# Optimization experiments

Hardware: AMD Instinct MI355X
Metric: run time of the kernel (lower is better)

Reference implementation:

```python
import jax, jax.numpy as jnp
import numpy as np

B, T, E, H, D = 4, 1024, 1024, 16, 64


def rel_shift(x):
    # x: [B, H, T1, T2] -> Transformer-XL relative shift
    b, h, t1, t2 = x.shape
    x = jnp.pad(x, ((0, 0), (0, 0), (0, 0), (1, 0)))  # pad zeros on left of last dim
    x = x.reshape(b, h, t2 + 1, t1)[:, :, 1:]
    return x.reshape(b, h, t1, t2)


def setup_inputs() -> dict:
    key = jax.random.key(0)
    ks = jax.random.split(key, 9)
    s = 0.02
    return {
        "x": jax.random.normal(ks[0], (B, T, E), jnp.float32),
        "pos": jax.random.normal(ks[1], (1, T, E), jnp.float32),
        "Wq": jax.random.normal(ks[2], (E, H, D), jnp.float32) * s,
        "Wk": jax.random.normal(ks[3], (E, H, D), jnp.float32) * s,
        "Wv": jax.random.normal(ks[4], (E, H, D), jnp.float32) * s,
        "Wr": jax.random.normal(ks[5], (E, H, D), jnp.float32) * s,
        "r_w_bias": jax.random.normal(ks[6], (1, H, 1, D), jnp.float32) * s,
        "r_r_bias": jax.random.normal(ks[7], (1, H, 1, D), jnp.float32) * s,
        "merge_W": jax.random.normal(ks[8], (E, E), jnp.float32) * s,
        "merge_b": jnp.zeros((E,), jnp.float32),
    }


def reference(x, pos, Wq, Wk, Wv, Wr, r_w_bias, r_r_bias, merge_W, merge_b):
    d = Wq.shape[-1]
    scale = d ** -0.5
    # per-head linear projections via einsum (MultiHeadLinear)
    q = jnp.einsum('bte,ehd->bhtd', x, Wq) * scale   # [B,H,T,D]
    k = jnp.einsum('bte,ehd->bhtd', x, Wk)           # [B,H,T,D]
    v = jnp.einsum('bte,ehd->bhtd', x, Wv)           # [B,H,T,D]
    r = jnp.einsum('upe,ehd->uhpd', pos, Wr)[0]      # [H,P,D], P == T

    # content logits: (q + u) . k
    content_logits = jnp.einsum('bhtd,bhsd->bhts', q + r_w_bias, k)
    # relative logits: (q + v_bias) . rel_keys, then rel_shift
    relative_logits = jnp.einsum('bhtd,hpd->bhtp', q + r_r_bias, r)
    relative_logits = rel_shift(relative_logits)

    logits = content_logits + relative_logits        # [B,H,T,T]
    weights = jax.nn.softmax(logits, axis=-1)
    # attend and merge heads: [B,T,H,D] -> [B,T,E]
    attended = jnp.einsum('bhts,bhsd->bthd', weights, v).reshape(x.shape[0], x.shape[1], -1)
    return attended @ merge_W + merge_b
```

## Files before the change

### kernel.cpp

```cpp
#include <hip/hip_runtime.h>
#include <hip/hip_bf16.h>

#define BB 4
#define TT 1024
#define EE 1024
#define HH 16
#define DD 64

typedef unsigned short ushort_t;
typedef unsigned int uint_t;
typedef __attribute__((ext_vector_type(8))) short short8;
typedef __attribute__((ext_vector_type(4))) float f32x4;

__device__ __forceinline__ ushort_t f2bf(float f) {
  uint_t u = __float_as_uint(f);
  u += 0x7fffu + ((u >> 16) & 1u);
  return (ushort_t)(u >> 16);
}
__device__ __forceinline__ float bf2f(ushort_t s) {
  return __uint_as_float(((uint_t)s) << 16);
}

__device__ __forceinline__ void gload16(const ushort_t* src, ushort_t* dst) {
  __builtin_amdgcn_global_load_lds(
      (const __attribute__((address_space(1))) void*)src,
      (__attribute__((address_space(3))) void*)dst, 16, 0, 0);
}

__global__ void __launch_bounds__(256) conv_flat(
    const float* __restrict__ in, ushort_t* __restrict__ out, int n) {
  int i = (blockIdx.x * 256 + threadIdx.x) * 8;
  if (i >= n) return;
  float4 a = *(const float4*)(in + i);
  float4 b = *(const float4*)(in + i + 4);
  uint4 o;
  o.x = (uint_t)f2bf(a.x) | ((uint_t)f2bf(a.y) << 16);
  o.y = (uint_t)f2bf(a.z) | ((uint_t)f2bf(a.w) << 16);
  o.z = (uint_t)f2bf(b.x) | ((uint_t)f2bf(b.y) << 16);
  o.w = (uint_t)f2bf(b.z) | ((uint_t)f2bf(b.w) << 16);
  *(uint4*)(out + i) = o;
}

__global__ void __launch_bounds__(256) trans_conv4(
    const float* __restrict__ W0, const float* __restrict__ W1,
    const float* __restrict__ W2, const float* __restrict__ W3,
    ushort_t* __restrict__ O0, ushort_t* __restrict__ O1,
    ushort_t* __restrict__ O2, ushort_t* __restrict__ O3) {
  const float* W; ushort_t* Oh;
  switch (blockIdx.z) {
    case 0: W = W0; Oh = O0; break;
    case 1: W = W1; Oh = O1; break;
    case 2: W = W2; Oh = O2; break;
    default: W = W3; Oh = O3; break;
  }
  __shared__ float Ts[64][65];
  const int n0 = blockIdx.x * 64, k0 = blockIdx.y * 64;
  const int t = threadIdx.x;
  const int r = t >> 2, cs = (t & 3) * 16;
  const float* src = W + (size_t)(k0 + r) * 1024 + n0 + cs;
  #pragma unroll
  for (int e = 0; e < 16; e += 4) {
    float4 v4 = *(const float4*)(src + e);
    Ts[r][cs + e] = v4.x; Ts[r][cs + e + 1] = v4.y;
    Ts[r][cs + e + 2] = v4.z; Ts[r][cs + e + 3] = v4.w;
  }
  __syncthreads();
  ushort_t hb[16];
  #pragma unroll
  for (int e = 0; e < 16; e++) hb[e] = f2bf(Ts[cs + e][r]);
  ushort_t* dh = Oh + (size_t)(n0 + r) * 1024 + k0 + cs;
  *(uint4*)dh = *(const uint4*)hb;
  *(uint4*)(dh + 8) = *(const uint4*)(hb + 8);
}

__global__ void __launch_bounds__(256) trans_conv(
    const float* __restrict__ W, ushort_t* __restrict__ Oh,
    ushort_t* __restrict__ Ol) {
  __shared__ float Ts[64][65];
  const int n0 = blockIdx.x * 64, k0 = blockIdx.y * 64;
  const int t = threadIdx.x;
  const int r = t >> 2, cs = (t & 3) * 16;
  const float* src = W + (size_t)(k0 + r) * 1024 + n0 + cs;
  #pragma unroll
  for (int e = 0; e < 16; e += 4) {
    float4 v4 = *(const float4*)(src + e);
    Ts[r][cs + e] = v4.x; Ts[r][cs + e + 1] = v4.y;
    Ts[r][cs + e + 2] = v4.z; Ts[r][cs + e + 3] = v4.w;
  }
  __syncthreads();
  ushort_t hb[16], lb[16];
  #pragma unroll
  for (int e = 0; e < 16; e++) {
    float v = Ts[cs + e][r];
    hb[e] = f2bf(v);
    lb[e] = f2bf(v - bf2f(hb[e]));
  }
  ushort_t* dh = Oh + (size_t)(n0 + r) * 1024 + k0 + cs;
  *(uint4*)dh = *(const uint4*)hb;
  *(uint4*)(dh + 8) = *(const uint4*)(hb + 8);
  ushort_t* dl = Ol + (size_t)(n0 + r) * 1024 + k0 + cs;
  *(uint4*)dl = *(const uint4*)lb;
  *(uint4*)(dl + 8) = *(const uint4*)(lb + 8);
}

__global__ void __launch_bounds__(256) mfma_gemm_proj(
    const ushort_t* __restrict__ A,
    const ushort_t* __restrict__ B0, const ushort_t* __restrict__ B1,
    const ushort_t* __restrict__ B2,
    ushort_t* __restrict__ o_qu, ushort_t* __restrict__ o_qv,
    ushort_t* __restrict__ o_k, ushort_t* __restrict__ o_v,
    const float* __restrict__ bias_u, const float* __restrict__ bias_v,
    int mode) {
  __shared__ ushort_t sA[2][128 * 32];
  __shared__ ushort_t sB[2][128 * 32];
  const int tid = threadIdx.x;
  const int w = tid >> 6, lane = tid & 63, g = lane >> 4, cl = lane & 15;
  const int wr = w >> 1, wc = w & 1;

  int widx, n0l;
  const ushort_t* Bt;
  if (mode == 0) {
    widx = blockIdx.x >> 3;
    n0l = (blockIdx.x & 7) * 128;
    Bt = (widx == 0) ? B0 : ((widx == 1) ? B1 : B2);
  } else {
    widx = 3;
    n0l = blockIdx.x * 128;
    Bt = B0;
  }
  const int m0 = blockIdx.y * 128;

  f32x4 acc[4][4];
  #pragma unroll
  for (int fi = 0; fi < 4; fi++)
    #pragma unroll
    for (int fj = 0; fj < 4; fj++) acc[fi][fj] = (f32x4){0.f, 0.f, 0.f, 0.f};

  auto STAGE = [&](int buf, int t) {
    const int k0b = t * 64;
    #pragma unroll
    for (int i = 0; i < 2; i++) {
      int cb = w * 128 + i * 64;
      int c = cb + lane;
      const char* sa = (const char*)A + (size_t)(m0 + (c >> 2)) * 2048 + k0b + (c & 3) * 16;
      gload16((const ushort_t*)sa, &sA[buf][cb * 8]);
      const char* sb = (const char*)Bt + (size_t)(n0l + (c >> 2)) * 2048 + k0b + (c & 3) * 16;
      gload16((const ushort_t*)sb, &sB[buf][cb * 8]);
    }
  };

  STAGE(0, 0);
  __syncthreads();
  int cur = 0;
  for (int t = 0; t < 32; t++) {
    if (t + 1 < 32) STAGE(cur ^ 1, t + 1);
    short8 af[4], bfr[4];
    #pragma unroll
    for (int f = 0; f < 4; f++) {
      af[f] = *(const short8*)&sA[cur][(wr * 64 + f * 16 + cl) * 32 + g * 8];
      bfr[f] = *(const short8*)&sB[cur][(wc * 64 + f * 16 + cl) * 32 + g * 8];
    }
    #pragma unroll
    for (int fi = 0; fi < 4; fi++)
      #pragma unroll
      for (int fj = 0; fj < 4; fj++)
        acc[fi][fj] = __builtin_amdgcn_mfma_f32_16x16x32_bf16(af[fi], bfr[fj], acc[fi][fj], 0, 0, 0);
    __syncthreads();
    cur ^= 1;
  }

  #pragma unroll
  for (int fi = 0; fi < 4; fi++)
    #pragma unroll
    for (int fj = 0; fj < 4; fj++)
      #pragma unroll
      for (int reg = 0; reg < 4; reg++) {
        int m = m0 + wr * 64 + fi * 16 + 4 * g + reg;
        int n = n0l + wc * 64 + fj * 16 + cl;
        float val = acc[fi][fj][reg];
        int h = n >> 6, d = n & 63;
        if (mode == 0) {
          int b = m >> 10, tt = m & 1023;
          if (widx == 0) {
            size_t idx = (((size_t)(b * HH + h)) * TT + tt) * DD + d;
            float s = val * 0.125f;
            o_qu[idx] = f2bf(s + bias_u[n]);
            o_qv[idx] = f2bf(s + bias_v[n]);
          } else if (widx == 1) {
            size_t idx = (((size_t)(b * HH + h)) * TT + tt) * DD + d;
            o_k[idx] = f2bf(val);
          } else {
            size_t idx = (((size_t)(b * HH + h)) * DD + d) * TT + tt;
            o_v[idx] = f2bf(val);
          }
        } else {
          size_t idx = ((size_t)h * TT + m) * DD + d;
          o_qu[idx] = f2bf(val);
        }
      }
}

__global__ void __launch_bounds__(256) mfma_gemm_merge(
    const ushort_t* __restrict__ Ah, const ushort_t* __restrict__ Al,
    const ushort_t* __restrict__ Bh, const ushort_t* __restrict__ Bl,
    const float* __restrict__ bias, float* __restrict__ out) {
  __shared__ ushort_t sAh[2][128 * 32], sAl[2][128 * 32];
  __shared__ ushort_t sBh[2][128 * 32], sBl[2][128 * 32];
  const int tid = threadIdx.x;
  const int w = tid >> 6, lane = tid & 63, g = lane >> 4, cl = lane & 15;
  const int wr = w >> 1, wc = w & 1;
  const int n0l = blockIdx.x * 128;
  const int m0 = blockIdx.y * 128;

  f32x4 acc[4][4];
  #pragma unroll
  for (int fi = 0; fi < 4; fi++)
    #pragma unroll
    for (int fj = 0; fj < 4; fj++) acc[fi][fj] = (f32x4){0.f, 0.f, 0.f, 0.f};

  auto STAGE = [&](int buf, int t) {
    const int k0b = t * 64;
    #pragma unroll
    for (int i = 0; i < 2; i++) {
      int cb = w * 128 + i * 64;
      int c = cb + lane;
      size_t offA = (size_t)(m0 + (c >> 2)) * 2048 + k0b + (c & 3) * 16;
      size_t offB = (size_t)(n0l + (c >> 2)) * 2048 + k0b + (c & 3) * 16;
      gload16((const ushort_t*)((const char*)Ah + offA), &sAh[buf][cb * 8]);
      gload16((const ushort_t*)((const char*)Al + offA), &sAl[buf][cb * 8]);
      gload16((const ushort_t*)((const char*)Bh + offB), &sBh[buf][cb * 8]);
      gload16((const ushort_t*)((const char*)Bl + offB), &sBl[buf][cb * 8]);
    }
  };

  STAGE(0, 0);
  __syncthreads();
  int cur = 0;
  for (int t = 0; t < 32; t++) {
    if (t + 1 < 32) STAGE(cur ^ 1, t + 1);
    short8 ah[4], al[4], bh[4], bl[4];
    #pragma unroll
    for (int f = 0; f < 4; f++) {
      int ra = (wr * 64 + f * 16 + cl) * 32 + g * 8;
      int rb = (wc * 64 + f * 16 + cl) * 32 + g * 8;
      ah[f] = *(const short8*)&sAh[cur][ra];
      al[f] = *(const short8*)&sAl[cur][ra];
      bh[f] = *(const short8*)&sBh[cur][rb];
      bl[f] = *(const short8*)&sBl[cur][rb];
    }
    #pragma unroll
    for (int fi = 0; fi < 4; fi++)
      #pragma unroll
      for (int fj = 0; fj < 4; fj++) {
        acc[fi][fj] = __builtin_amdgcn_mfma_f32_16x16x32_bf16(ah[fi], bh[fj], acc[fi][fj], 0, 0, 0);
        acc[fi][fj] = __builtin_amdgcn_mfma_f32_16x16x32_bf16(al[fi], bh[fj], acc[fi][fj], 0, 0, 0);
        acc[fi][fj] = __builtin_amdgcn_mfma_f32_16x16x32_bf16(ah[fi], bl[fj], acc[fi][fj], 0, 0, 0);
      }
    __syncthreads();
    cur ^= 1;
  }

  #pragma unroll
  for (int fi = 0; fi < 4; fi++)
    #pragma unroll
    for (int fj = 0; fj < 4; fj++)
      #pragma unroll
      for (int reg = 0; reg < 4; reg++) {
        int m = m0 + wr * 64 + fi * 16 + 4 * g + reg;
        int n = n0l + wc * 64 + fj * 16 + cl;
        out[(size_t)m * 1024 + n] = acc[fi][fj][reg] + bias[n];
      }
}

__device__ __forceinline__ void stage8s(ushort_t* region, const ushort_t* grow0,
                                        int rstride, int r0, int lane) {
  int flat16 = r0 * 8 + lane;
  int row = flat16 >> 3;
  int ch = flat16 & 7;
  const ushort_t* src = grow0 + (size_t)row * rstride + ((((ch << 4) ^ ((row & 7) << 4))) >> 1);
  gload16(src, region + r0 * 64);
}

__device__ __forceinline__ short8 ldsw(const ushort_t* base, int row, int offB) {
  const char* p = (const char*)base + row * 128 + (offB ^ ((row & 7) << 4));
  return *(const short8*)p;
}

__global__ void __launch_bounds__(256, 3) attn_mfma_kernel(
    const ushort_t* __restrict__ qu_g, const ushort_t* __restrict__ qv_g,
    const ushort_t* __restrict__ k_g, const ushort_t* __restrict__ vt_g,
    const ushort_t* __restrict__ r_g,
    ushort_t* __restrict__ att_h, ushort_t* __restrict__ att_l)
{
    __shared__ ushort_t sK[2][64 * 64];
    __shared__ ushort_t sVt[2][64 * 64];
    __shared__ ushort_t sG[4][2304];

    const int tid = threadIdx.x;
    const int w = tid >> 6;
    const int lane = tid & 63;
    const int g = lane >> 4;
    const int cl = lane & 15;

    const int lid = blockIdx.x + 16 * blockIdx.y + 256 * blockIdx.z;
    const int xcd = lid & 7, seq = lid >> 3;
    const int bhg = xcd * 8 + (seq >> 4);
    const int i0 = (seq & 15) * 64;
    const int h = bhg & 15;
    const int b = bhg >> 4;
    const size_t base_bh = ((size_t)(b * HH + h)) * TT * DD;
    const ushort_t* rh = r_g + (size_t)h * TT * DD;

    ushort_t* Gw = sG[w];
    ushort_t* Pb = sG[w];

    const int qrow = i0 + 16 * w + cl;
    const ushort_t* qup = qu_g + base_bh + (size_t)qrow * 64;
    short8 aQ0 = *(const short8*)(qup + 8 * g);
    short8 aQ1 = *(const short8*)(qup + 32 + 8 * g);
    const ushort_t* qv1p = qv_g + base_bh + (size_t)qrow * 64;
    short8 aV0 = *(const short8*)(qv1p + 8 * g);
    short8 aV1 = *(const short8*)(qv1p + 32 + 8 * g);
    int r2row = qrow + 1; if (r2row > 1023) r2row = 1023;
    const ushort_t* qv2p = qv_g + base_bh + (size_t)r2row * 64;
    short8 aV0s = *(const short8*)(qv2p + 8 * g);
    short8 aV1s = *(const short8*)(qv2p + 32 + 8 * g);

    auto STAGE = [&](int bufi, int jt16) {
      const ushort_t* kb = k_g + base_bh + (size_t)(jt16 * 64) * 64;
      stage8s(sK[bufi], kb, 64, 16 * w, lane);
      stage8s(sK[bufi], kb, 64, 16 * w + 8, lane);
      const ushort_t* vtb = vt_g + base_bh + (size_t)(jt16 * 64);
      stage8s(sVt[bufi], vtb, 1024, 16 * w, lane);
      stage8s(sVt[bufi], vtb, 1024, 16 * w + 8, lane);
    };

    auto RLD = [&](int base, int s, short8& A, short8& B) {
      const ushort_t* rp = rh + (size_t)(base + s * 16 + cl) * 64 + 8 * g;
      A = *(const short8*)rp;
      B = *(const short8*)(rp + 32);
    };
    auto GST = [&](int s, short8 A, short8 B, short8 X0, short8 X1) {
      f32x4 ga = (f32x4){0.f, 0.f, 0.f, 0.f};
      ga = __builtin_amdgcn_mfma_f32_16x16x32_bf16(X0, A, ga, 0, 0, 0);
      ga = __builtin_amdgcn_mfma_f32_16x16x32_bf16(X1, B, ga, 0, 0, 0);
      int m = s * 16 + cl;
      *(uint_t*)(Gw + m * 18 + 4 * g) =
          (uint_t)f2bf(ga[0]) | ((uint_t)f2bf(ga[1]) << 16);
      *(uint_t*)(Gw + m * 18 + 4 * g + 2) =
          (uint_t)f2bf(ga[2]) | ((uint_t)f2bf(ga[3]) << 16);
    };

    f32x4 Oa[4];
    #pragma unroll
    for (int q = 0; q < 4; q++) Oa[q] = (f32x4){0.f, 0.f, 0.f, 0.f};
    float lrun[4] = {0.f, 0.f, 0.f, 0.f};

    STAGE(0, 0);
    __syncthreads();
    int cur = 0;

    for (int jt16 = 0; jt16 < 16; jt16++) {
        const int j0 = jt16 * 64;
        const int dji = j0 - i0;

        f32x4 sacc[4];
        #pragma unroll
        for (int jt = 0; jt < 4; jt++) sacc[jt] = (f32x4){0.f, 0.f, 0.f, 0.f};
        __builtin_amdgcn_s_setprio(1);
        #pragma unroll
        for (int jt = 0; jt < 4; jt++) {
            int krow = jt * 16 + cl;
            short8 b0 = ldsw(sK[cur], krow, 16 * g);
            short8 b1 = ldsw(sK[cur], krow, 64 + 16 * g);
            sacc[jt] = __builtin_amdgcn_mfma_f32_16x16x32_bf16(aQ0, b0, sacc[jt], 0, 0, 0);
            sacc[jt] = __builtin_amdgcn_mfma_f32_16x16x32_bf16(aQ1, b1, sacc[jt], 0, 0, 0);
        }
        __builtin_amdgcn_s_setprio(0);

        if (dji < 0) {
            const int cbase1w = 1008 + dji - 16 * w;
            short8 a0, b0, a1, b1, a2, b2;
            RLD(cbase1w, 0, a0, b0);
            RLD(cbase1w, 1, a1, b1);
            RLD(cbase1w, 2, a2, b2);
            GST(0, a0, b0, aV0, aV1); RLD(cbase1w, 3, a0, b0);
            GST(1, a1, b1, aV0, aV1); RLD(cbase1w, 4, a1, b1);
            GST(2, a2, b2, aV0, aV1);
            GST(3, a0, b0, aV0, aV1);
            GST(4, a1, b1, aV0, aV1);
            if (jt16 + 1 < 16) STAGE(cur ^ 1, jt16 + 1);
            #pragma unroll
            for (int jt = 0; jt < 4; jt++)
                #pragma unroll
                for (int reg = 0; reg < 4; reg++) {
                    int m1p = 15 + jt * 16 + cl - 4 * g - reg;
                    sacc[jt][reg] += bf2f(Gw[m1p * 18 + 4 * g + reg]);
                }
        } else if (dji > 0) {
            int rbase2w = dji - 17 - 16 * w;
            if (rbase2w < 0) rbase2w = 0;
            short8 a0, b0, a1, b1, a2, b2;
            RLD(rbase2w, 0, a0, b0);
            RLD(rbase2w, 1, a1, b1);
            RLD(rbase2w, 2, a2, b2);
            GST(0, a0, b0, aV0s, aV1s); RLD(rbase2w, 3, a0, b0);
            GST(1, a1, b1, aV0s, aV1s); RLD(rbase2w, 4, a1, b1);
            GST(2, a2, b2, aV0s, aV1s);
            GST(3, a0, b0, aV0s, aV1s);
            GST(4, a1, b1, aV0s, aV1s);
            if (jt16 + 1 < 16) STAGE(cur ^ 1, jt16 + 1);
            #pragma unroll
            for (int jt = 0; jt < 4; jt++)
                #pragma unroll
                for (int reg = 0; reg < 4; reg++) {
                    int dlt = dji + jt * 16 + cl - 16 * w - 4 * g - reg;
                    int idx2 = dlt - 2 - rbase2w;
                    if (dlt >= 2) sacc[jt][reg] += bf2f(Gw[idx2 * 18 + 4 * g + reg]);
                }
        } else {
            ushort_t* Gw2 = Gw + 64 * 18;
            for (int sub = 0; sub < 4; sub++) {
                int m = sub * 16 + cl;
                const ushort_t* rp = rh + (size_t)(960 + m) * 64 + 8 * g;
                f32x4 gacc = (f32x4){0.f, 0.f, 0.f, 0.f};
                gacc = __builtin_amdgcn_mfma_f32_16x16x32_bf16(aV0, *(const short8*)rp, gacc, 0, 0, 0);
                gacc = __builtin_amdgcn_mfma_f32_16x16x32_bf16(aV1, *(const short8*)(rp + 32), gacc, 0, 0, 0);
                *(uint_t*)(Gw + m * 18 + 4 * g) =
                    (uint_t)f2bf(gacc[0]) | ((uint_t)f2bf(gacc[1]) << 16);
                *(uint_t*)(Gw + m * 18 + 4 * g + 2) =
                    (uint_t)f2bf(gacc[2]) | ((uint_t)f2bf(gacc[3]) << 16);
            }
            for (int sub = 0; sub < 4; sub++) {
                int m = sub * 16 + cl;
                const ushort_t* rp = rh + (size_t)m * 64 + 8 * g;
                f32x4 gacc = (f32x4){0.f, 0.f, 0.f, 0.f};
                gacc = __builtin_amdgcn_mfma_f32_16x16x32_bf16(aV0s, *(const short8*)rp, gacc, 0, 0, 0);
                gacc = __builtin_amdgcn_mfma_f32_16x16x32_bf16(aV1s, *(const short8*)(rp + 32), gacc, 0, 0, 0);
                *(uint_t*)(Gw2 + m * 18 + 4 * g) =
                    (uint_t)f2bf(gacc[0]) | ((uint_t)f2bf(gacc[1]) << 16);
                *(uint_t*)(Gw2 + m * 18 + 4 * g + 2) =
                    (uint_t)f2bf(gacc[2]) | ((uint_t)f2bf(gacc[3]) << 16);
            }
            if (jt16 + 1 < 16) STAGE(cur ^ 1, jt16 + 1);
            #pragma unroll
            for (int jt = 0; jt < 4; jt++)
                #pragma unroll
                for (int reg = 0; reg < 4; reg++) {
                    int m1 = 63 + jt * 16 + cl - 16 * w - 4 * g - reg;
                    if (m1 <= 63) sacc[jt][reg] += bf2f(Gw[m1 * 18 + 4 * g + reg]);
                }
            #pragma unroll
            for (int jt = 0; jt < 4; jt++)
                #pragma unroll
                for (int reg = 0; reg < 4; reg++) {
                    int dlt = jt * 16 + cl - 16 * w - 4 * g - reg;
                    if (dlt >= 2) sacc[jt][reg] += bf2f(Gw2[(dlt - 2) * 18 + 4 * g + reg]);
                }
        }

        #pragma unroll
        for (int reg = 0; reg < 4; reg++) {
            #pragma unroll
            for (int jt = 0; jt < 4; jt++) {
                float p = __expf(sacc[jt][reg]);
                lrun[reg] += p;
                Pb[(4 * g + reg) * 72 + jt * 16 + cl] = f2bf(p);
            }
        }

        __builtin_amdgcn_s_setprio(1);
        #pragma unroll
        for (int kk = 0; kk < 2; kk++) {
            short8 aP = *(const short8*)((const char*)Pb + cl * 144 + 64 * kk + 16 * g);
            #pragma unroll
            for (int q = 0; q < 4; q++) {
                short8 bV = ldsw(sVt[cur], q * 16 + cl, kk * 64 + 16 * g);
                Oa[q] = __builtin_amdgcn_mfma_f32_16x16x32_bf16(aP, bV, Oa[q], 0, 0, 0);
            }
        }
        __builtin_amdgcn_s_setprio(0);

        __syncthreads();
        cur ^= 1;
    }

    float inv[4];
    #pragma unroll
    for (int reg = 0; reg < 4; reg++) {
        float s = lrun[reg];
        #pragma unroll
        for (int msk = 1; msk <= 8; msk <<= 1) s += __shfl_xor(s, msk);
        inv[reg] = 1.f / s;
    }
    #pragma unroll
    for (int q = 0; q < 4; q++)
        #pragma unroll
        for (int reg = 0; reg < 4; reg++) {
            int i = i0 + 16 * w + 4 * g + reg;
            int d = q * 16 + cl;
            float val = Oa[q][reg] * inv[reg];
            ushort_t hi = f2bf(val);
            ushort_t lo = f2bf(val - bf2f(hi));
            size_t oi = (((size_t)(b * TT + i)) * HH + h) * DD + d;
            att_h[oi] = hi;
            att_l[oi] = lo;
        }
}

extern "C" void kernel_launch(void* const* d_in, const int* in_sizes, int n_in,
                              void* d_out, int out_size, void* d_ws, size_t ws_size,
                              hipStream_t stream) {
    const float* x    = (const float*)d_in[0];
    const float* pos  = (const float*)d_in[1];
    const float* Wq   = (const float*)d_in[2];
    const float* Wk   = (const float*)d_in[3];
    const float* Wv   = (const float*)d_in[4];
    const float* Wr   = (const float*)d_in[5];
    const float* ub   = (const float*)d_in[6];
    const float* vb   = (const float*)d_in[7];
    const float* mW   = (const float*)d_in[8];
    const float* mb   = (const float*)d_in[9];
    float* out = (float*)d_out;

    const size_t M1 = 1u << 20;
    ushort_t* ws = (ushort_t*)d_ws;
    ushort_t* xb   = ws;
    ushort_t* posb = ws + 4 * M1;
    ushort_t* wqt  = ws + 5 * M1;
    ushort_t* wkt  = ws + 6 * M1;
    ushort_t* wvt  = ws + 7 * M1;
    ushort_t* wrt  = ws + 8 * M1;
    ushort_t* wmh  = ws + 9 * M1;
    ushort_t* wml  = ws + 10 * M1;
    ushort_t* qu_g = ws + 11 * M1;
    ushort_t* qv_g = ws + 15 * M1;
    ushort_t* k_g  = ws + 19 * M1;
    ushort_t* vt_g = ws + 23 * M1;
    ushort_t* r_g  = ws + 27 * M1;
    ushort_t* ath  = ws + 28 * M1;
    ushort_t* atl  = ws + 32 * M1;

    dim3 blk(256);

    hipLaunchKernelGGL(conv_flat, dim3(2048), blk, 0, stream, x, xb, 4194304);
    hipLaunchKernelGGL(conv_flat, dim3(512), blk, 0, stream, pos, posb, 1048576);
    hipLaunchKernelGGL(trans_conv4, dim3(16, 16, 4), blk, 0, stream,
                       Wq, Wk, Wv, Wr, wqt, wkt, wvt, wrt);
    hipLaunchKernelGGL(trans_conv, dim3(16, 16), blk, 0, stream, mW, wmh, wml);

    hipLaunchKernelGGL(mfma_gemm_proj, dim3(24, 32), blk, 0, stream,
                       xb, wqt, wkt, wvt, qu_g, qv_g, k_g, vt_g, ub, vb, 0);
    hipLaunchKernelGGL(mfma_gemm_proj, dim3(8, 8), blk, 0, stream,
                       posb, wrt, wrt, wrt, r_g, r_g, r_g, r_g, ub, vb, 1);

    hipLaunchKernelGGL(attn_mfma_kernel, dim3(TT / 64, HH, BB), blk, 0, stream,
                       qu_g, qv_g, k_g, vt_g, r_g, ath, atl);

    hipLaunchKernelGGL(mfma_gemm_merge, dim3(8, 32), blk, 0, stream,
                       ath, atl, wmh, wml, mb, out);
}
```

Baseline: 301.8 us.

## Load K and V fragments directly from global memory instead of LDS staging

Removes the double-buffered LDS staging of K and transposed V tiles and the per-iteration block barrier. Each wave now loads its MFMA operand fragments directly from global memory, and launch bounds are raised to allow four blocks per CU. This aims to cut LDS footprint and synchronisation overhead, at the cost of redundant global/L2 reads across waves and no prefetch overlap of the next tile.

```diff
diff --git a/kernel.cpp b/kernel.cpp
--- a/kernel.cpp
+++ b/kernel.cpp
@@ -272,28 +272,12 @@
       }
 }
 
-__device__ __forceinline__ void stage8s(ushort_t* region, const ushort_t* grow0,
-                                        int rstride, int r0, int lane) {
-  int flat16 = r0 * 8 + lane;
-  int row = flat16 >> 3;
-  int ch = flat16 & 7;
-  const ushort_t* src = grow0 + (size_t)row * rstride + ((((ch << 4) ^ ((row & 7) << 4))) >> 1);
-  gload16(src, region + r0 * 64);
-}
-
-__device__ __forceinline__ short8 ldsw(const ushort_t* base, int row, int offB) {
-  const char* p = (const char*)base + row * 128 + (offB ^ ((row & 7) << 4));
-  return *(const short8*)p;
-}
-
-__global__ void __launch_bounds__(256, 3) attn_mfma_kernel(
+__global__ void __launch_bounds__(256, 4) attn_mfma_kernel(
     const ushort_t* __restrict__ qu_g, const ushort_t* __restrict__ qv_g,
     const ushort_t* __restrict__ k_g, const ushort_t* __restrict__ vt_g,
     const ushort_t* __restrict__ r_g,
     ushort_t* __restrict__ att_h, ushort_t* __restrict__ att_l)
 {
-    __shared__ ushort_t sK[2][64 * 64];
-    __shared__ ushort_t sVt[2][64 * 64];
     __shared__ ushort_t sG[4][2304];
 
     const int tid = threadIdx.x;
@@ -325,15 +309,6 @@
     const ushort_t* qv2p = qv_g + base_bh + (size_t)r2row * 64;
     short8 aV0s = *(const short8*)(qv2p + 8 * g);
     short8 aV1s = *(const short8*)(qv2p + 32 + 8 * g);
-
-    auto STAGE = [&](int bufi, int jt16) {
-      const ushort_t* kb = k_g + base_bh + (size_t)(jt16 * 64) * 64;
-      stage8s(sK[bufi], kb, 64, 16 * w, lane);
-      stage8s(sK[bufi], kb, 64, 16 * w + 8, lane);
-      const ushort_t* vtb = vt_g + base_bh + (size_t)(jt16 * 64);
-      stage8s(sVt[bufi], vtb, 1024, 16 * w, lane);
-      stage8s(sVt[bufi], vtb, 1024, 16 * w + 8, lane);
-    };
 
     auto RLD = [&](int base, int s, short8& A, short8& B) {
       const ushort_t* rp = rh + (size_t)(base + s * 16 + cl) * 64 + 8 * g;
@@ -356,10 +331,6 @@
     for (int q = 0; q < 4; q++) Oa[q] = (f32x4){0.f, 0.f, 0.f, 0.f};
     float lrun[4] = {0.f, 0.f, 0.f, 0.f};
 
-    STAGE(0, 0);
-    __syncthreads();
-    int cur = 0;
-
     for (int jt16 = 0; jt16 < 16; jt16++) {
         const int j0 = jt16 * 64;
         const int dji = j0 - i0;
@@ -370,11 +341,11 @@
         __builtin_amdgcn_s_setprio(1);
         #pragma unroll
         for (int jt = 0; jt < 4; jt++) {
-            int krow = jt * 16 + cl;
-            short8 b0 = ldsw(sK[cur], krow, 16 * g);
-            short8 b1 = ldsw(sK[cur], krow, 64 + 16 * g);
-            sacc[jt] = __builtin_amdgcn_mfma_f32_16x16x32_bf16(aQ0, b0, sacc[jt], 0, 0, 0);
-            sacc[jt] = __builtin_amdgcn_mfma_f32_16x16x32_bf16(aQ1, b1, sacc[jt], 0, 0, 0);
+            const ushort_t* kp = k_g + base_bh + (size_t)(j0 + jt * 16 + cl) * 64 + 8 * g;
+            short8 kb0 = *(const short8*)kp;
+            short8 kb1 = *(const short8*)(kp + 32);
+            sacc[jt] = __builtin_amdgcn_mfma_f32_16x16x32_bf16(aQ0, kb0, sacc[jt], 0, 0, 0);
+            sacc[jt] = __builtin_amdgcn_mfma_f32_16x16x32_bf16(aQ1, kb1, sacc[jt], 0, 0, 0);
         }
         __builtin_amdgcn_s_setprio(0);
 
@@ -389,7 +360,6 @@
             GST(2, a2, b2, aV0, aV1);
             GST(3, a0, b0, aV0, aV1);
             GST(4, a1, b1, aV0, aV1);
-            if (jt16 + 1 < 16) STAGE(cur ^ 1, jt16 + 1);
             #pragma unroll
             for (int jt = 0; jt < 4; jt++)
                 #pragma unroll
@@ -409,7 +379,6 @@
             GST(2, a2, b2, aV0s, aV1s);
             GST(3, a0, b0, aV0s, aV1s);
             GST(4, a1, b1, aV0s, aV1s);
-            if (jt16 + 1 < 16) STAGE(cur ^ 1, jt16 + 1);
             #pragma unroll
             for (int jt = 0; jt < 4; jt++)
                 #pragma unroll
@@ -442,7 +411,6 @@
                 *(uint_t*)(Gw2 + m * 18 + 4 * g + 2) =
                     (uint_t)f2bf(gacc[2]) | ((uint_t)f2bf(gacc[3]) << 16);
             }
-            if (jt16 + 1 < 16) STAGE(cur ^ 1, jt16 + 1);
             #pragma unroll
             for (int jt = 0; jt < 4; jt++)
                 #pragma unroll
@@ -475,14 +443,13 @@
             short8 aP = *(const short8*)((const char*)Pb + cl * 144 + 64 * kk + 16 * g);
             #pragma unroll
             for (int q = 0; q < 4; q++) {
-                short8 bV = ldsw(sVt[cur], q * 16 + cl, kk * 64 + 16 * g);
+                const ushort_t* vp = vt_g + base_bh + (size_t)(q * 16 + cl) * 1024
+                                     + j0 + kk * 32 + 8 * g;
+                short8 bV = *(const short8*)vp;
                 Oa[q] = __builtin_amdgcn_mfma_f32_16x16x32_bf16(aP, bV, Oa[q], 0, 0, 0);
             }
         }
         __builtin_amdgcn_s_setprio(0);
-
-        __syncthreads();
-        cur ^= 1;
     }
 
     float inv[4];
```

Result: slower. 356.7 us (+18.2%).
